# Kernel optimization log

Measured on AMD Instinct MI355X. Metric: run time of the kernel, lower is better.

Reference implementation:

```python
import jax, jax.numpy as jnp
import numpy as np

C_IN = 2048
C_HID = 1024
C_EMB = 256


def setup_inputs() -> dict:
    key = jax.random.key(0)
    ks = jax.random.split(key, 14)
    B, T = 4, 2048
    sc = 0.02  # keep logits in a sane range for softmax
    inp = {
        "x": jax.random.normal(ks[0], (B, T, C_IN), jnp.float32) * 0.05,
        "theta_w": jax.random.normal(ks[1], (C_HID, C_IN), jnp.float32) * sc,
        "theta_b": jnp.zeros((C_HID,), jnp.float32),
        "phi_w": jax.random.normal(ks[2], (C_HID, C_IN), jnp.float32) * sc,
        "phi_b": jnp.zeros((C_HID,), jnp.float32),
        "g_w": jax.random.normal(ks[3], (C_HID, C_IN), jnp.float32) * sc,
        "g_b": jnp.zeros((C_HID,), jnp.float32),
        "rou_w": jax.random.normal(ks[4], (2,), jnp.float32),
        "rou_b": jnp.zeros((1,), jnp.float32),
        "w_w": jax.random.normal(ks[5], (C_IN, C_HID), jnp.float32) * sc,
        "w_b": jnp.zeros((C_IN,), jnp.float32),
        "emb_w": jax.random.normal(ks[6], (C_EMB, C_IN), jnp.float32) * sc,
        "emb_b": jnp.zeros((C_EMB,), jnp.float32),
        "B": B,
        "T": T,
    }
    return inp


def reference(x, theta_w, theta_b, phi_w, phi_b, g_w, g_b, rou_w, rou_b,
              w_w, w_b, emb_w, emb_b, B, T):
    x = x.reshape(B, T, C_IN)
    # NSSM: raw self-similarity + softmax over last dim -> (B, T, T)
    nssm = jax.nn.softmax(jnp.einsum('btc,bsc->bts', x, x), axis=-1)
    xc = jnp.swapaxes(x, 1, 2)  # (B, C_IN, T), channels-first like Conv1d
    # 1x1 Conv1d == per-timestep linear over channels
    x_theta = jnp.einsum('oc,bct->bot', theta_w, xc) + theta_b[None, :, None]  # (B,H,T)
    x_phi = jnp.einsum('oc,bct->bto', phi_w, xc) + phi_b[None, None, :]        # (B,T,H)
    att = jax.nn.softmax(jnp.einsum('bth,bhs->bts', x_phi, x_theta), axis=-1)  # (B,T,T)
    # Faithful to torch.cat(dim=0).view(B,-1,T,T): row-major interleave of batches
    cat = jnp.concatenate([nssm, att], axis=0).reshape(B, 2, T, T)
    # rou: 1x1 Conv2d(2->1) == weighted sum of the two maps + bias, then softmax
    moca = jax.nn.softmax(rou_w[0] * cat[:, 0] + rou_w[1] * cat[:, 1] + rou_b[0], axis=-1)  # (B,T,T)
    x_g = jnp.einsum('oc,bct->bot', g_w, xc) + g_b[None, :, None]  # (B,H,T)
    y = jnp.einsum('bht,bts->bhs', x_g, moca)                      # (B,H,T)
    wz = jnp.einsum('oh,bht->bot', w_w, y) + w_b[None, :, None]    # (B,C_IN,T)
    z = jnp.swapaxes(wz + xc, 1, 2)                                # (B,T,C_IN)
    return z @ emb_w.T + emb_b                                     # (B,T,256)
```

## Files before the change

### kernel.cpp

```cpp
#include <hip/hip_runtime.h>
#include <hip/hip_bf16.h>

constexpr int kB   = 4;
constexpr int kT   = 2048;
constexpr int kCIN = 2048;
constexpr int kHID = 1024;
constexpr int kEMB = 256;

typedef __bf16 bf16_t;
typedef __bf16 bf16x8 __attribute__((ext_vector_type(8)));
typedef __bf16 bf16x4 __attribute__((ext_vector_type(4)));
typedef float  f32x4  __attribute__((ext_vector_type(4)));

__device__ __forceinline__ void gll16(const void* g, void* l) {
  auto lp = reinterpret_cast<__attribute__((address_space(3))) uint32_t*>(
      reinterpret_cast<uintptr_t>(l));
  __builtin_amdgcn_global_load_lds(static_cast<const uint32_t*>(g), lp, 16, 0, 0);
}

#define MFMA_BF16 __builtin_amdgcn_mfma_f32_16x16x32_bf16

template <int MODE>
__device__ __forceinline__ void gemm256(bf16_t* lds, const bf16_t* A, const bf16_t* B,
                                        void* Cv, int lda, int ldb, int ldc,
                                        int m0, int n0, int Klen, const float* biasN) {
  const int tid  = threadIdx.x;
  const int lane = tid & 63, wv = tid >> 6;
  const int wm = wv & 1, wn = wv >> 1;
  const int lm = lane & 15, q = lane >> 4;
  const int l8 = lane >> 3;
  const int slot = (lane & 7) ^ l8;

  bf16_t* const sA = lds;
  bf16_t* const sB = lds + 32768;

  int aoff[4], boff[4];
#pragma unroll
  for (int cc = 0; cc < 4; cc++) {
    const int ra = cc * 64 + wv * 8 + l8;
    aoff[cc] = ra * lda;
    const int nb = ((ra >> 5) & 3) * 64 + (ra >> 7) * 32 + (ra & 31);
    boff[cc] = nb * ldb;
  }
  const bf16_t* const Ab = A + (size_t)m0 * lda + slot * 8;
  const bf16_t* const Bb = B + (size_t)n0 * ldb + slot * 8;

  const int x0 = ((q ^ (lm & 7)) << 3);
  const int x1 = (((q + 4) ^ (lm & 7)) << 3);

#define STAGE_A(T, H)                                                         \
  {                                                                           \
    bf16_t* dst_ = sA + (((T) & 1) << 14);                                    \
    const bf16_t* src_ = Ab + ((T) << 6);                                     \
    gll16(src_ + aoff[(H)], dst_ + ((H) << 12) + (wv << 9));                  \
    gll16(src_ + aoff[2 + (H)], dst_ + ((2 + (H)) << 12) + (wv << 9));        \
  }
#define STAGE_B(T, G)                                                         \
  {                                                                           \
    bf16_t* dst_ = sB + (((T) & 1) << 14);                                    \
    const bf16_t* src_ = Bb + ((T) << 6);                                     \
    gll16(src_ + boff[2 * (G)], dst_ + ((2 * (G)) << 12) + (wv << 9));        \
    gll16(src_ + boff[2 * (G) + 1], dst_ + ((2 * (G) + 1) << 12) + (wv << 9));\
  }
#define READ_A(BUF, H)                                                        \
  _Pragma("unroll") for (int i = 0; i < 4; i++) {                             \
    const bf16_t* p_ = (BUF) + ((wm * 128 + (H) * 64 + i * 16 + lm) << 6);    \
    af[i][0] = *(const bf16x8*)(p_ + x0);                                     \
    af[i][1] = *(const bf16x8*)(p_ + x1);                                     \
  }
#define READ_B(BF, BUF, G)                                                    \
  _Pragma("unroll") for (int j2 = 0; j2 < 2; j2++) {                          \
    const bf16_t* p_ = (BUF) + (((G) * 128 + wn * 32 + j2 * 16 + lm) << 6);   \
    BF[j2][0] = *(const bf16x8*)(p_ + x0);                                    \
    BF[j2][1] = *(const bf16x8*)(p_ + x1);                                    \
  }
#define QUAD(H, G, BF)                                                        \
  _Pragma("unroll") for (int i2 = 0; i2 < 4; i2++)                            \
  _Pragma("unroll") for (int j2 = 0; j2 < 2; j2++)                            \
  _Pragma("unroll") for (int kk = 0; kk < 2; kk++)                            \
    acc[(H) * 4 + i2][(G) * 2 + j2] = MFMA_BF16(                              \
        af[i2][kk], BF[j2][kk], acc[(H) * 4 + i2][(G) * 2 + j2], 0, 0, 0);
#define MFMA_OPEN()                                                           \
  asm volatile("s_waitcnt lgkmcnt(0)" ::: "memory");                          \
  __builtin_amdgcn_s_setprio(1);
#define MFMA_CLOSE() __builtin_amdgcn_s_setprio(0);

  f32x4 acc[8][4];
#pragma unroll
  for (int i = 0; i < 8; i++)
#pragma unroll
    for (int j = 0; j < 4; j++)
#pragma unroll
      for (int r = 0; r < 4; r++) acc[i][j][r] = 0.f;

  const int nt = Klen >> 6;

  STAGE_A(0, 0) STAGE_B(0, 0) STAGE_B(0, 1) STAGE_A(0, 1)
  STAGE_A(1, 0) STAGE_B(1, 0) STAGE_B(1, 1) STAGE_A(1, 1)
  asm volatile("s_waitcnt vmcnt(8)" ::: "memory");
  __builtin_amdgcn_s_barrier();

  bf16x8 af[4][2], bf0[2][2], bf1[2][2];
  for (int t = 0; t < nt; t++) {
    bf16_t* const a = sA + ((t & 1) << 14);
    bf16_t* const b = sB + ((t & 1) << 14);
    const bool pf = (t + 2) < nt;
    READ_A(a, 0)
    READ_B(bf0, b, 0)
    asm volatile("s_waitcnt lgkmcnt(8)" ::: "memory");
    __builtin_amdgcn_s_barrier();
    MFMA_OPEN()
    QUAD(0, 0, bf0)
    MFMA_CLOSE()
    __builtin_amdgcn_s_barrier();
    READ_B(bf1, b, 1)
    if (pf) STAGE_A(t + 2, 0)
    __builtin_amdgcn_s_barrier();
    MFMA_OPEN()
    QUAD(0, 1, bf1)
    MFMA_CLOSE()
    __builtin_amdgcn_s_barrier();
    READ_A(a, 1)
    if (pf) STAGE_B(t + 2, 0)
    __builtin_amdgcn_s_barrier();
    MFMA_OPEN()
    QUAD(1, 1, bf1)
    MFMA_CLOSE()
    __builtin_amdgcn_s_barrier();
    if (pf) { STAGE_B(t + 2, 1) STAGE_A(t + 2, 1) }
    __builtin_amdgcn_s_barrier();
    __builtin_amdgcn_s_setprio(1);
    QUAD(1, 0, bf0)
    __builtin_amdgcn_s_setprio(0);
    if (pf)
      asm volatile("s_waitcnt vmcnt(8)" ::: "memory");
    else if (t + 1 < nt)
      asm volatile("s_waitcnt vmcnt(0)" ::: "memory");
    __builtin_amdgcn_s_barrier();
  }

#pragma unroll
  for (int i = 0; i < 8; i++) {
    const int gm = m0 + wm * 128 + (i >> 2) * 64 + (i & 3) * 16 + q * 4;
#pragma unroll
    for (int j = 0; j < 4; j++) {
      const int gn = n0 + wn * 64 + j * 16 + lm;
      const float bn_ = biasN ? biasN[gn] : 0.f;
#pragma unroll
      for (int r = 0; r < 4; r++) {
        const float v = acc[i][j][r] + bn_;
        const size_t idx = (size_t)(gm + r) * ldc + gn;
        if (MODE == 0) ((bf16_t*)Cv)[idx] = (bf16_t)v;
        else           ((float*)Cv)[idx] = v;
      }
    }
  }
#undef STAGE_A
#undef STAGE_B
#undef READ_A
#undef READ_B
#undef QUAD
#undef MFMA_OPEN
#undef MFMA_CLOSE
}

__device__ __forceinline__ bool mirror_is_late(int z, int qq, int p) {
  const int R = qq >> 2, C = p >> 2;
  const int local = 8 * R - (R * (R - 1)) / 2 + (C - R);
  return (z == 3) && (local >= 16);
}

__global__ __launch_bounds__(256) void k_prep(const float* __restrict__ x,
                                              const float* __restrict__ th,
                                              const float* __restrict__ ph,
                                              const float* __restrict__ g,
                                              const float* __restrict__ emb,
                                              const float* __restrict__ w_w,
                                              const float* __restrict__ w_b,
                                              const float* __restrict__ emb_b,
                                              const float* __restrict__ tb,
                                              const float* __restrict__ pb,
                                              const float* __restrict__ gb,
                                              bf16_t* __restrict__ xbf,
                                              bf16_t* __restrict__ wqkv,
                                              bf16_t* __restrict__ embbf,
                                              bf16_t* __restrict__ wwT,
                                              float* __restrict__ biase,
                                              float* __restrict__ bqkv) {
  __shared__ float tile[64 * 66];
  const int b = blockIdx.x;
  if (b < 23040) {
    const float* in; bf16_t* o; long i;
    if (b < 16384)      { in = x;   o = xbf;                            i = (long)b * 256 + threadIdx.x; }
    else if (b < 18432) { in = th;  o = wqkv;                           i = (long)(b - 16384) * 256 + threadIdx.x; }
    else if (b < 20480) { in = ph;  o = wqkv + (size_t)kHID * kCIN;     i = (long)(b - 18432) * 256 + threadIdx.x; }
    else if (b < 22528) { in = g;   o = wqkv + (size_t)2 * kHID * kCIN; i = (long)(b - 20480) * 256 + threadIdx.x; }
    else                { in = emb; o = embbf;                          i = (long)(b - 22528) * 256 + threadIdx.x; }
    float4 v = ((const float4*)in)[i];
    bf16x4 ov;
    ov[0] = (bf16_t)v.x; ov[1] = (bf16_t)v.y; ov[2] = (bf16_t)v.z; ov[3] = (bf16_t)v.w;
    ((bf16x4*)o)[i] = ov;
  } else if (b < 23552) {
    int j = b - 23040;
    int h0 = (j & 15) * 64, c0 = (j >> 4) * 64;
#pragma unroll
    for (int k = 0; k < 16; k++) {
      int e = k * 256 + threadIdx.x;
      int r = e >> 6, c = e & 63;
      tile[r * 66 + c] = w_w[(size_t)(c0 + r) * kHID + h0 + c];
    }
    __syncthreads();
#pragma unroll
    for (int k = 0; k < 16; k++) {
      int e = k * 256 + threadIdx.x;
      int r = e >> 6, c = e & 63;
      wwT[(size_t)(h0 + r) * kCIN + c0 + c] = (bf16_t)tile[c * 66 + r];
    }
  } else if (b < 23808) {
    int e = b - 23552;
    float acc = 0.f;
    for (int c = threadIdx.x; c < kCIN; c += 256)
      acc += emb[(size_t)e * kCIN + c] * w_b[c];
#pragma unroll
    for (int o = 32; o > 0; o >>= 1) acc += __shfl_xor(acc, o, 64);
    __syncthreads();
    if ((threadIdx.x & 63) == 0) tile[threadIdx.x >> 6] = acc;
    __syncthreads();
    if (threadIdx.x == 0) biase[e] = tile[0] + tile[1] + tile[2] + tile[3] + emb_b[e];
  } else {
    int i = (b - 23808) * 256 + threadIdx.x;
    if (i < 3072)
      bqkv[i] = i < 1024 ? tb[i] : (i < 2048 ? pb[i - 1024] : gb[i - 2048]);
  }
}

__global__ __launch_bounds__(512, 2) void k_mega1(const bf16_t* __restrict__ xbf,
                                                  const bf16_t* __restrict__ wqkv,
                                                  const bf16_t* __restrict__ embbf,
                                                  const bf16_t* __restrict__ wwT,
                                                  bf16_t* __restrict__ xtphi,
                                                  bf16_t* __restrict__ S1,
                                                  bf16_t* __restrict__ Mbf,
                                                  const float* __restrict__ bqkv,
                                                  float* __restrict__ S1f) {
  __shared__ bf16_t lds[65536];
  const int bid = blockIdx.x;
  if (bid < 384) {
    const int bm = bid & 31, bn = bid >> 5;
    gemm256<0>(lds, xbf, wqkv, xtphi, 2048, 2048, 3072,
               bm * 256, bn * 256, 2048, bqkv);
  } else if (bid < 508) {
    int s = bid - 384;
    const int z = s / 36;
    int tt = s % 36, rr = 0;
    while (tt >= 8 - rr) { tt -= 8 - rr; rr++; }
    const bf16_t* Az = xbf + (size_t)z * kT * kCIN;
    gemm256<0>(lds, Az, Az, S1 + (size_t)z * kT * kT, 2048, 2048, 2048,
               rr * 256, (rr + tt) * 256, 2048, nullptr);
  } else if (bid < 512) {
    const int m = bid - 508;
    gemm256<0>(lds, embbf, wwT, Mbf, 2048, 2048, 1024, 0, m * 256, 2048, nullptr);
  } else {
    const int qj = bid - 512;
    const int s = 124 + (qj >> 2), ks = qj & 3;
    const int z = s / 36;
    int tt = s % 36, rr = 0;
    while (tt >= 8 - rr) { tt -= 8 - rr; rr++; }
    const bf16_t* Az = xbf + (size_t)z * kT * kCIN;
    gemm256<1>(lds, Az + (size_t)(rr * 256) * 2048 + ks * 512,
               Az + (size_t)((rr + tt) * 256) * 2048 + ks * 512,
               S1f + (size_t)qj * 65536, 2048, 2048, 256, 0, 0, 512, nullptr);
  }
}

__global__ __launch_bounds__(512, 2) void k_gemm2(const bf16_t* __restrict__ xtphi,
                                                  bf16_t* __restrict__ S2,
                                                  const float* __restrict__ S1f,
                                                  bf16_t* __restrict__ S1,
                                                  const bf16_t* __restrict__ Mbf,
                                                  float* __restrict__ Wf) {
  __shared__ bf16_t lds[65536];
  const int bid = blockIdx.x;
  if (bid < 256) {
    const int bm = bid & 7, bn = (bid >> 3) & 7, z = bid >> 6;
    const bf16_t* base = xtphi + (size_t)z * kT * 3072;
    gemm256<0>(lds, base + 1024, base, S2 + (size_t)z * kT * kT, 3072, 3072, 2048,
               bm * 256, bn * 256, 1024, nullptr);
  } else if (bid < 320) {
    const int wj = bid - 256;
    const int tle = wj & 31, ks = wj >> 5;
    const int z = tle >> 3, ntile = tle & 7;
    gemm256<1>(lds, Mbf + ks * 512,
               xtphi + (size_t)(z * kT + ntile * 256) * 3072 + 2048 + ks * 512,
               Wf + (size_t)(ks * 32 + tle) * 65536, 1024, 3072, 256, 0, 0, 512,
               nullptr);
  } else if (bid < 640) {
    const int cb = bid - 320;
    const int t20 = cb >> 4, part = cb & 15;
    const int s = 124 + t20;
    const int z = s / 36;
    int tt = s % 36, rr = 0;
    while (tt >= 8 - rr) { tt -= 8 - rr; rr++; }
    const float* base = S1f + (size_t)(4 * t20) * 65536;
    const int e0 = part * 4096 + threadIdx.x * 8;
    f32x4 lo = *(const f32x4*)(base + e0);
    f32x4 hi = *(const f32x4*)(base + e0 + 4);
#pragma unroll
    for (int ks = 1; ks < 4; ks++) {
      const float* p = base + (size_t)ks * 65536 + e0;
      f32x4 l2 = *(const f32x4*)p, h2 = *(const f32x4*)(p + 4);
#pragma unroll
      for (int k = 0; k < 4; k++) { lo[k] += l2[k]; hi[k] += h2[k]; }
    }
    const int r = e0 >> 8, c = e0 & 255;
    bf16x8 o;
#pragma unroll
    for (int k = 0; k < 4; k++) { o[k] = (bf16_t)lo[k]; o[4 + k] = (bf16_t)hi[k]; }
    *(bf16x8*)(S1 + (size_t)z * kT * kT + (size_t)(rr * 256 + r) * kT + (rr + tt) * 256 + c) = o;
  } else {
    int j = bid - 640;
    int z = j / 496, t = j % 496, qq = 0;
    while (t >= 31 - qq) { t -= 31 - qq; qq++; }
    int p = qq + 1 + t;
    if (mirror_is_late(z, qq, p)) return;
    bf16_t* tile = lds;
    const size_t base = (size_t)z * kT * kT;
#pragma unroll
    for (int k = 0; k < 8; k++) {
      int e = k * 512 + threadIdx.x;
      int r = e >> 6, c = e & 63;
      tile[r * 66 + c] = S1[base + (size_t)(qq * 64 + r) * kT + p * 64 + c];
    }
    __syncthreads();
#pragma unroll
    for (int k = 0; k < 8; k++) {
      int e = k * 512 + threadIdx.x;
      int r = e >> 6, c = e & 63;
      S1[base + (size_t)(p * 64 + r) * kT + qq * 64 + c] = tile[c * 66 + r];
    }
  }
}

__global__ __launch_bounds__(256) void k_util2(bf16_t* __restrict__ S1,
                                               const float* __restrict__ Wf,
                                               bf16_t* __restrict__ W) {
  __shared__ bf16_t tile[64 * 66];
  const int bid = blockIdx.x;
  if (bid < 1984) {
    int j = bid;
    int z = j / 496, t = j % 496, qq = 0;
    while (t >= 31 - qq) { t -= 31 - qq; qq++; }
    int p = qq + 1 + t;
    if (!mirror_is_late(z, qq, p)) return;
    const size_t base = (size_t)z * kT * kT;
#pragma unroll
    for (int k = 0; k < 16; k++) {
      int e = k * 256 + threadIdx.x;
      int r = e >> 6, c = e & 63;
      tile[r * 66 + c] = S1[base + (size_t)(qq * 64 + r) * kT + p * 64 + c];
    }
    __syncthreads();
#pragma unroll
    for (int k = 0; k < 16; k++) {
      int e = k * 256 + threadIdx.x;
      int r = e >> 6, c = e & 63;
      S1[base + (size_t)(p * 64 + r) * kT + qq * 64 + c] = tile[c * 66 + r];
    }
  } else {
    const long i = (long)(bid - 1984) * 2048 + threadIdx.x * 8;
    const int tle = (int)(i >> 16), w = (int)(i & 65535);
    const float* a = Wf + (size_t)tle * 65536 + w;
    const float* b = a + (size_t)32 * 65536;
    f32x4 lo = *(const f32x4*)a, hi = *(const f32x4*)(a + 4);
    f32x4 l2 = *(const f32x4*)b, h2 = *(const f32x4*)(b + 4);
    const int e = w >> 8, sl = w & 255;
    bf16x8 o;
#pragma unroll
    for (int k = 0; k < 4; k++) {
      o[k]     = (bf16_t)(lo[k] + l2[k]);
      o[4 + k] = (bf16_t)(hi[k] + h2[k]);
    }
    *(bf16x8*)(W + (size_t)(tle >> 3) * kEMB * kT + (size_t)e * kT + (tle & 7) * 256 + sl) = o;
  }
}

__global__ __launch_bounds__(256) void k_moca(const bf16_t* __restrict__ S1,
                                              const bf16_t* __restrict__ S2,
                                              bf16_t* __restrict__ dst,
                                              const float* __restrict__ rou_w,
                                              const float* __restrict__ rou_b) {
  const int wv = threadIdx.x >> 6, lane = threadIdx.x & 63;
  const int t = blockIdx.x * 4 + wv, b = blockIdx.y;
  const size_t T2 = (size_t)kT * kT;
  const bf16_t* src = (b < 2) ? S1 : S2;
  const int pb = (b < 2) ? 2 * b : 2 * (b - 2);
  const bf16_t* rA = src + (size_t)pb * T2 + (size_t)t * kT;
  const bf16_t* rB = rA + T2;

  float va[32], vb[32];
#pragma unroll
  for (int c = 0; c < 4; c++) {
    bf16x8 a  = *(const bf16x8*)(rA + c * 512 + lane * 8);
    bf16x8 bb = *(const bf16x8*)(rB + c * 512 + lane * 8);
#pragma unroll
    for (int k = 0; k < 8; k++) { va[c * 8 + k] = (float)a[k]; vb[c * 8 + k] = (float)bb[k]; }
  }
  auto wmax = [](float v) {
#pragma unroll
    for (int o = 32; o > 0; o >>= 1) v = fmaxf(v, __shfl_xor(v, o, 64));
    return v;
  };
  auto wsum = [](float v) {
#pragma unroll
    for (int o = 32; o > 0; o >>= 1) v += __shfl_xor(v, o, 64);
    return v;
  };

  float m = -1e30f, s;
#pragma unroll
  for (int j = 0; j < 32; j++) m = fmaxf(m, va[j]);
  m = wmax(m); s = 0.f;
#pragma unroll
  for (int j = 0; j < 32; j++) { va[j] = __expf(va[j] - m); s += va[j]; }
  const float invA = 1.f / wsum(s);

  m = -1e30f;
#pragma unroll
  for (int j = 0; j < 32; j++) m = fmaxf(m, vb[j]);
  m = wmax(m); s = 0.f;
#pragma unroll
  for (int j = 0; j < 32; j++) { vb[j] = __expf(vb[j] - m); s += vb[j]; }
  const float invB = 1.f / wsum(s);

  const float r0 = rou_w[0], r1 = rou_w[1], rb2 = rou_b[0];
#pragma unroll
  for (int j = 0; j < 32; j++) va[j] = r0 * va[j] * invA + r1 * vb[j] * invB + rb2;

  m = -1e30f;
#pragma unroll
  for (int j = 0; j < 32; j++) m = fmaxf(m, va[j]);
  m = wmax(m); s = 0.f;
#pragma unroll
  for (int j = 0; j < 32; j++) { va[j] = __expf(va[j] - m); s += va[j]; }
  const float invC = 1.f / wsum(s);

  bf16_t* o = dst + (size_t)b * T2 + (size_t)t * kT;
#pragma unroll
  for (int c = 0; c < 4; c++) {
    bf16x8 ov;
#pragma unroll
    for (int k = 0; k < 8; k++) ov[k] = (bf16_t)(va[c * 8 + k] * invC);
    *(bf16x8*)(o + c * 512 + lane * 8) = ov;
  }
}

__global__ __launch_bounds__(256) void k_mocaT(const bf16_t* __restrict__ in,
                                               bf16_t* __restrict__ out) {
  __shared__ bf16_t tile[64 * 66];
  size_t base = (size_t)blockIdx.z * kT * kT;
  int r0 = blockIdx.y * 64, c0 = blockIdx.x * 64;
#pragma unroll
  for (int k = 0; k < 16; k++) {
    int e = k * 256 + threadIdx.x;
    int r = e >> 6, c = e & 63;
    tile[r * 66 + c] = in[base + (size_t)(r0 + r) * kT + c0 + c];
  }
  __syncthreads();
#pragma unroll
  for (int k = 0; k < 16; k++) {
    int e = k * 256 + threadIdx.x;
    int r = e >> 6, c = e & 63;
    out[base + (size_t)(c0 + r) * kT + r0 + c] = tile[c * 66 + r];
  }
}

__global__ __launch_bounds__(512, 2) void k_outq(const bf16_t* __restrict__ mocaT,
                                                 const bf16_t* __restrict__ W,
                                                 const bf16_t* __restrict__ xbf,
                                                 const bf16_t* __restrict__ embbf,
                                                 float* __restrict__ outf) {
  __shared__ bf16_t lds[65536];
  const int bid = blockIdx.x;
  const int m = bid & 31, ks = bid >> 5;
  float* Cv = outf + (size_t)ks * 2097152 + (size_t)m * 65536;
  if (ks < 4) {
    const int z = m >> 3;
    gemm256<1>(lds,
               mocaT + (size_t)z * kT * kT + (size_t)((m & 7) * 256) * kT + ks * 512,
               W + (size_t)z * kEMB * kT + ks * 512,
               Cv, 2048, 2048, 256, 0, 0, 512, nullptr);
  } else {
    gemm256<1>(lds,
               xbf + (size_t)(m * 256) * kCIN + (ks - 4) * 512,
               embbf + (ks - 4) * 512,
               Cv, 2048, 2048, 256, 0, 0, 512, nullptr);
  }
}

__global__ __launch_bounds__(256) void k_fin(const float* __restrict__ outf,
                                             const float* __restrict__ biase,
                                             float* __restrict__ out) {
  const long i = (long)blockIdx.x * 2048 + threadIdx.x * 8;
  const int e0 = (int)(i & 255);
  f32x4 lo = {0.f, 0.f, 0.f, 0.f}, hi = {0.f, 0.f, 0.f, 0.f};
#pragma unroll
  for (int ks = 0; ks < 8; ks++) {
    const float* p = outf + (size_t)ks * 2097152 + i;
    f32x4 l2 = *(const f32x4*)p, h2 = *(const f32x4*)(p + 4);
#pragma unroll
    for (int k = 0; k < 4; k++) { lo[k] += l2[k]; hi[k] += h2[k]; }
  }
#pragma unroll
  for (int k = 0; k < 4; k++) {
    lo[k] += biase[e0 + k];
    hi[k] += biase[e0 + 4 + k];
  }
  *(f32x4*)(out + i) = lo;
  *(f32x4*)(out + i + 4) = hi;
}

extern "C" void kernel_launch(void* const* d_in, const int* in_sizes, int n_in,
                              void* d_out, int out_size, void* d_ws, size_t ws_size,
                              hipStream_t stream) {
  const float* x       = (const float*)d_in[0];
  const float* theta_w = (const float*)d_in[1];
  const float* theta_b = (const float*)d_in[2];
  const float* phi_w   = (const float*)d_in[3];
  const float* phi_b   = (const float*)d_in[4];
  const float* g_w     = (const float*)d_in[5];
  const float* g_b     = (const float*)d_in[6];
  const float* rou_w   = (const float*)d_in[7];
  const float* rou_b   = (const float*)d_in[8];
  const float* w_w     = (const float*)d_in[9];
  const float* w_b     = (const float*)d_in[10];
  const float* emb_w   = (const float*)d_in[11];
  const float* emb_b   = (const float*)d_in[12];
  float* out = (float*)d_out;

  char* ws = (char*)d_ws;
  size_t off = 0;
  auto alloc = [&](size_t bytes) -> char* {
    off = (off + 255) & ~(size_t)255;
    char* p = ws + off;
    off += bytes;
    return p;
  };

  const size_t BT = (size_t)kB * kT;
  const size_t T2 = (size_t)kT * kT;

  bf16_t* xbf   = (bf16_t*)alloc(BT * kCIN * 2);
  bf16_t* wqkv  = (bf16_t*)alloc((size_t)3 * kHID * kCIN * 2);
  bf16_t* embbf = (bf16_t*)alloc((size_t)kEMB * kCIN * 2);
  bf16_t* wwT   = (bf16_t*)alloc((size_t)kHID * kCIN * 2);
  bf16_t* xtphi = (bf16_t*)alloc(BT * 3072 * 2);
  float*  Wf    = (float*)alloc((size_t)64 * 65536 * 4);
  bf16_t* mocab = (bf16_t*)alloc((size_t)kB * T2 * 2);
  bf16_t* Mbf   = (bf16_t*)alloc((size_t)kEMB * kHID * 2);
  bf16_t* W     = (bf16_t*)alloc((size_t)kB * kEMB * kT * 2);
  float*  biase = (float*)alloc((size_t)kEMB * 4);
  float*  bqkv  = (float*)alloc((size_t)3072 * 4);
  bf16_t* S1    = (bf16_t*)alloc((size_t)kB * T2 * 2);
  bf16_t* S2    = (bf16_t*)alloc((size_t)kB * T2 * 2);
  bf16_t* mocaT = (bf16_t*)xtphi;
  float*  S1f   = (float*)mocab;
  float*  outf  = (float*)S1;

  k_prep<<<dim3(23820), 256, 0, stream>>>(x, theta_w, phi_w, g_w, emb_w, w_w, w_b,
                                          emb_b, theta_b, phi_b, g_b,
                                          xbf, wqkv, embbf, wwT, biase, bqkv);
  k_mega1<<<dim3(592), 512, 0, stream>>>(xbf, wqkv, embbf, wwT, xtphi, S1, Mbf,
                                         bqkv, S1f);
  k_gemm2<<<dim3(2624), 512, 0, stream>>>(xtphi, S2, S1f, S1, Mbf, Wf);
  k_util2<<<dim3(3008), 256, 0, stream>>>(S1, Wf, W);
  k_moca<<<dim3(kT / 4, kB), 256, 0, stream>>>(S1, S2, mocab, rou_w, rou_b);
  k_mocaT<<<dim3(32, 32, kB), 256, 0, stream>>>(mocab, mocaT);
  k_outq<<<dim3(256), 512, 0, stream>>>(mocaT, W, xbf, embbf, outf);
  k_fin<<<dim3(1024), 256, 0, stream>>>(outf, biase, out);
}
```

Baseline: 416.7 us.

## Rebalance split-K gram tiles across kernels and halve output split-K

Moves the split-K self-similarity tile GEMMs from the first mega-kernel into the second GEMM kernel, so they run alongside the attention-logit GEMM. Their reduction, together with the mirrored transpose writes, moves into the utility kernel, which now fuses reduce, store and mirror per 64x64 sub-tile. The final output GEMM drops from 8-way to 4-way split-K (K=1024 per block, 128 blocks), which halves partial-sum traffic in the finisher at the cost of fewer, longer blocks on a large GPU. The aim is better load balance across launches and less fp32 scratch traffic.

```diff
diff --git a/kernel.cpp b/kernel.cpp
--- a/kernel.cpp
+++ b/kernel.cpp
@@ -241,8 +241,7 @@
                                                   bf16_t* __restrict__ xtphi,
                                                   bf16_t* __restrict__ S1,
                                                   bf16_t* __restrict__ Mbf,
-                                                  const float* __restrict__ bqkv,
-                                                  float* __restrict__ S1f) {
+                                                  const float* __restrict__ bqkv) {
   __shared__ bf16_t lds[65536];
   const int bid = blockIdx.x;
   if (bid < 384) {
@@ -257,28 +256,18 @@
     const bf16_t* Az = xbf + (size_t)z * kT * kCIN;
     gemm256<0>(lds, Az, Az, S1 + (size_t)z * kT * kT, 2048, 2048, 2048,
                rr * 256, (rr + tt) * 256, 2048, nullptr);
-  } else if (bid < 512) {
+  } else {
     const int m = bid - 508;
     gemm256<0>(lds, embbf, wwT, Mbf, 2048, 2048, 1024, 0, m * 256, 2048, nullptr);
-  } else {
-    const int qj = bid - 512;
-    const int s = 124 + (qj >> 2), ks = qj & 3;
-    const int z = s / 36;
-    int tt = s % 36, rr = 0;
-    while (tt >= 8 - rr) { tt -= 8 - rr; rr++; }
-    const bf16_t* Az = xbf + (size_t)z * kT * kCIN;
-    gemm256<1>(lds, Az + (size_t)(rr * 256) * 2048 + ks * 512,
-               Az + (size_t)((rr + tt) * 256) * 2048 + ks * 512,
-               S1f + (size_t)qj * 65536, 2048, 2048, 256, 0, 0, 512, nullptr);
   }
 }
 
 __global__ __launch_bounds__(512, 2) void k_gemm2(const bf16_t* __restrict__ xtphi,
                                                   bf16_t* __restrict__ S2,
-                                                  const float* __restrict__ S1f,
-                                                  bf16_t* __restrict__ S1,
                                                   const bf16_t* __restrict__ Mbf,
-                                                  float* __restrict__ Wf) {
+                                                  float* __restrict__ Wf,
+                                                  const bf16_t* __restrict__ xbf,
+                                                  float* __restrict__ S1f) {
   __shared__ bf16_t lds[65536];
   const int bid = blockIdx.x;
   if (bid < 256) {
@@ -294,65 +283,81 @@
                xtphi + (size_t)(z * kT + ntile * 256) * 3072 + 2048 + ks * 512,
                Wf + (size_t)(ks * 32 + tle) * 65536, 1024, 3072, 256, 0, 0, 512,
                nullptr);
-  } else if (bid < 640) {
-    const int cb = bid - 320;
-    const int t20 = cb >> 4, part = cb & 15;
+  } else {
+    const int qj = bid - 320;
+    const int s = 124 + (qj >> 2), ks = qj & 3;
+    const int z = s / 36;
+    int tt = s % 36, rr = 0;
+    while (tt >= 8 - rr) { tt -= 8 - rr; rr++; }
+    const bf16_t* Az = xbf + (size_t)z * kT * kCIN;
+    gemm256<1>(lds, Az + (size_t)(rr * 256) * 2048 + ks * 512,
+               Az + (size_t)((rr + tt) * 256) * 2048 + ks * 512,
+               S1f + (size_t)qj * 65536, 2048, 2048, 256, 0, 0, 512, nullptr);
+  }
+}
+
+__global__ __launch_bounds__(256) void k_util2(bf16_t* __restrict__ S1,
+                                               const float* __restrict__ S1f,
+                                               const float* __restrict__ Wf,
+                                               bf16_t* __restrict__ W) {
+  __shared__ bf16_t tile[64 * 66];
+  const int bid = blockIdx.x;
+  const size_t T2 = (size_t)kT * kT;
+  if (bid < 320) {
+    const int t20 = bid >> 4, sb = bid & 15;
+    const int sr = sb >> 2, sc = sb & 3;
     const int s = 124 + t20;
     const int z = s / 36;
     int tt = s % 36, rr = 0;
     while (tt >= 8 - rr) { tt -= 8 - rr; rr++; }
-    const float* base = S1f + (size_t)(4 * t20) * 65536;
-    const int e0 = part * 4096 + threadIdx.x * 8;
-    f32x4 lo = *(const f32x4*)(base + e0);
-    f32x4 hi = *(const f32x4*)(base + e0 + 4);
-#pragma unroll
-    for (int ks = 1; ks < 4; ks++) {
-      const float* p = base + (size_t)ks * 65536 + e0;
-      f32x4 l2 = *(const f32x4*)p, h2 = *(const f32x4*)(p + 4);
-#pragma unroll
-      for (int k = 0; k < 4; k++) { lo[k] += l2[k]; hi[k] += h2[k]; }
-    }
-    const int r = e0 >> 8, c = e0 & 255;
-    bf16x8 o;
-#pragma unroll
-    for (int k = 0; k < 4; k++) { o[k] = (bf16_t)lo[k]; o[4 + k] = (bf16_t)hi[k]; }
-    *(bf16x8*)(S1 + (size_t)z * kT * kT + (size_t)(rr * 256 + r) * kT + (rr + tt) * 256 + c) = o;
-  } else {
-    int j = bid - 640;
+    const int cc = rr + tt;
+    if (tt == 0 && sr > sc) return;
+    const int r = threadIdx.x >> 2, c0 = (threadIdx.x & 3) << 4;
+    const float* base = S1f + (size_t)(4 * t20) * 65536 +
+                        (size_t)(sr * 64 + r) * 256 + sc * 64 + c0;
+    float v[16];
+#pragma unroll
+    for (int k = 0; k < 16; k++) v[k] = 0.f;
+#pragma unroll
+    for (int ks = 0; ks < 4; ks++) {
+      const float* p = base + (size_t)ks * 65536;
+#pragma unroll
+      for (int q4 = 0; q4 < 4; q4++) {
+        f32x4 t4 = *(const f32x4*)(p + q4 * 4);
+#pragma unroll
+        for (int k = 0; k < 4; k++) v[q4 * 4 + k] += t4[k];
+      }
+    }
+    bf16x8 o0, o1;
+#pragma unroll
+    for (int k = 0; k < 8; k++) { o0[k] = (bf16_t)v[k]; o1[k] = (bf16_t)v[8 + k]; }
+    const size_t zb = (size_t)z * T2;
+    bf16_t* up = S1 + zb + (size_t)(rr * 256 + sr * 64 + r) * kT + cc * 256 + sc * 64 + c0;
+    *(bf16x8*)up = o0;
+    *(bf16x8*)(up + 8) = o1;
+    if (tt == 0 && sr == sc) return;
+#pragma unroll
+    for (int k = 0; k < 8; k++) {
+      tile[r * 66 + c0 + k]     = o0[k];
+      tile[r * 66 + c0 + 8 + k] = o1[k];
+    }
+    __syncthreads();
+    bf16x8 w0, w1;
+#pragma unroll
+    for (int k = 0; k < 8; k++) {
+      w0[k] = tile[(c0 + k) * 66 + r];
+      w1[k] = tile[(c0 + 8 + k) * 66 + r];
+    }
+    bf16_t* lo = S1 + zb + (size_t)(cc * 256 + sc * 64 + r) * kT + rr * 256 + sr * 64 + c0;
+    *(bf16x8*)lo = w0;
+    *(bf16x8*)(lo + 8) = w1;
+  } else if (bid < 2304) {
+    int j = bid - 320;
     int z = j / 496, t = j % 496, qq = 0;
     while (t >= 31 - qq) { t -= 31 - qq; qq++; }
     int p = qq + 1 + t;
     if (mirror_is_late(z, qq, p)) return;
-    bf16_t* tile = lds;
-    const size_t base = (size_t)z * kT * kT;
-#pragma unroll
-    for (int k = 0; k < 8; k++) {
-      int e = k * 512 + threadIdx.x;
-      int r = e >> 6, c = e & 63;
-      tile[r * 66 + c] = S1[base + (size_t)(qq * 64 + r) * kT + p * 64 + c];
-    }
-    __syncthreads();
-#pragma unroll
-    for (int k = 0; k < 8; k++) {
-      int e = k * 512 + threadIdx.x;
-      int r = e >> 6, c = e & 63;
-      S1[base + (size_t)(p * 64 + r) * kT + qq * 64 + c] = tile[c * 66 + r];
-    }
-  }
-}
-
-__global__ __launch_bounds__(256) void k_util2(bf16_t* __restrict__ S1,
-                                               const float* __restrict__ Wf,
-                                               bf16_t* __restrict__ W) {
-  __shared__ bf16_t tile[64 * 66];
-  const int bid = blockIdx.x;
-  if (bid < 1984) {
-    int j = bid;
-    int z = j / 496, t = j % 496, qq = 0;
-    while (t >= 31 - qq) { t -= 31 - qq; qq++; }
-    int p = qq + 1 + t;
-    if (!mirror_is_late(z, qq, p)) return;
-    const size_t base = (size_t)z * kT * kT;
+    const size_t base = (size_t)z * T2;
 #pragma unroll
     for (int k = 0; k < 16; k++) {
       int e = k * 256 + threadIdx.x;
@@ -367,7 +372,7 @@
       S1[base + (size_t)(p * 64 + r) * kT + qq * 64 + c] = tile[c * 66 + r];
     }
   } else {
-    const long i = (long)(bid - 1984) * 2048 + threadIdx.x * 8;
+    const long i = (long)(bid - 2304) * 2048 + threadIdx.x * 8;
     const int tle = (int)(i >> 16), w = (int)(i & 65535);
     const float* a = Wf + (size_t)tle * 65536 + w;
     const float* b = a + (size_t)32 * 65536;
@@ -481,19 +486,22 @@
                                                  float* __restrict__ outf) {
   __shared__ bf16_t lds[65536];
   const int bid = blockIdx.x;
-  const int m = bid & 31, ks = bid >> 5;
-  float* Cv = outf + (size_t)ks * 2097152 + (size_t)m * 65536;
-  if (ks < 4) {
+  if (bid < 64) {
+    const int m = bid & 31, kh = bid >> 5;
     const int z = m >> 3;
     gemm256<1>(lds,
-               mocaT + (size_t)z * kT * kT + (size_t)((m & 7) * 256) * kT + ks * 512,
-               W + (size_t)z * kEMB * kT + ks * 512,
-               Cv, 2048, 2048, 256, 0, 0, 512, nullptr);
+               mocaT + (size_t)z * kT * kT + (size_t)((m & 7) * 256) * kT + kh * 1024,
+               W + (size_t)z * kEMB * kT + kh * 1024,
+               outf + (size_t)kh * 2097152 + (size_t)m * 65536,
+               2048, 2048, 256, 0, 0, 1024, nullptr);
   } else {
+    const int r = bid - 64;
+    const int m = r & 31, kh = r >> 5;
     gemm256<1>(lds,
-               xbf + (size_t)(m * 256) * kCIN + (ks - 4) * 512,
-               embbf + (ks - 4) * 512,
-               Cv, 2048, 2048, 256, 0, 0, 512, nullptr);
+               xbf + (size_t)(m * 256) * kCIN + kh * 1024,
+               embbf + kh * 1024,
+               outf + (size_t)(2 + kh) * 2097152 + (size_t)m * 65536,
+               2048, 2048, 256, 0, 0, 1024, nullptr);
   }
 }
 
@@ -504,7 +512,7 @@
   const int e0 = (int)(i & 255);
   f32x4 lo = {0.f, 0.f, 0.f, 0.f}, hi = {0.f, 0.f, 0.f, 0.f};
 #pragma unroll
-  for (int ks = 0; ks < 8; ks++) {
+  for (int ks = 0; ks < 4; ks++) {
     const float* p = outf + (size_t)ks * 2097152 + i;
     f32x4 l2 = *(const f32x4*)p, h2 = *(const f32x4*)(p + 4);
 #pragma unroll
@@ -569,12 +577,11 @@
   k_prep<<<dim3(23820), 256, 0, stream>>>(x, theta_w, phi_w, g_w, emb_w, w_w, w_b,
                                           emb_b, theta_b, phi_b, g_b,
                                           xbf, wqkv, embbf, wwT, biase, bqkv);
-  k_mega1<<<dim3(592), 512, 0, stream>>>(xbf, wqkv, embbf, wwT, xtphi, S1, Mbf,
-                                         bqkv, S1f);
-  k_gemm2<<<dim3(2624), 512, 0, stream>>>(xtphi, S2, S1f, S1, Mbf, Wf);
-  k_util2<<<dim3(3008), 256, 0, stream>>>(S1, Wf, W);
+  k_mega1<<<dim3(512), 512, 0, stream>>>(xbf, wqkv, embbf, wwT, xtphi, S1, Mbf, bqkv);
+  k_gemm2<<<dim3(400), 512, 0, stream>>>(xtphi, S2, Mbf, Wf, xbf, S1f);
+  k_util2<<<dim3(3328), 256, 0, stream>>>(S1, S1f, Wf, W);
   k_moca<<<dim3(kT / 4, kB), 256, 0, stream>>>(S1, S2, mocab, rou_w, rou_b);
   k_mocaT<<<dim3(32, 32, kB), 256, 0, stream>>>(mocab, mocaT);
-  k_outq<<<dim3(256), 512, 0, stream>>>(mocaT, W, xbf, embbf, outf);
+  k_outq<<<dim3(128), 512, 0, stream>>>(mocaT, W, xbf, embbf, outf);
   k_fin<<<dim3(1024), 256, 0, stream>>>(outf, biase, out);
 }
```

After: 410.8 us. No clear change (-1.4%).
